# Kernel optimization log

Hardware: AMD Instinct MI355X
Metric: run time of the kernel (lower is better)

Reference implementation:

```python
import jax, jax.numpy as jnp
import numpy as np

N, IN_DIM, H, D = 4096, 512, 8, 64
NEG = -1e9  # additive mask value for non-edges


def setup_inputs() -> dict:
    key = jax.random.key(0)
    k1, k2, k3, k4, k5, k6 = jax.random.split(key, 6)
    data = jax.random.normal(k1, (N, IN_DIM), dtype=jnp.float32)
    r = jax.random.uniform(k2, (N, N), dtype=jnp.float32)
    connectivity = jnp.where(r < 0.05, 0.0, NEG).astype(jnp.float32)
    # xavier-uniform-ish init for params
    lim_w = float(np.sqrt(6.0 / (IN_DIM + H * D)))
    W = jax.random.uniform(k3, (H * D, IN_DIM), jnp.float32, -lim_w, lim_w)
    b = jnp.zeros((H * D,), jnp.float32)
    lim_p = float(np.sqrt(6.0 / (H * D + 1)))
    src_proj = jax.random.uniform(k4, (1, H, D), jnp.float32, -lim_p, lim_p)
    trg_proj = jax.random.uniform(k5, (1, H, D), jnp.float32, -lim_p, lim_p)
    return {"data": data, "connectivity": connectivity, "W": W, "b": b,
            "src_proj": src_proj, "trg_proj": trg_proj}


def reference(data, connectivity, W, b, src_proj, trg_proj):
    # dropout is identity in eval mode (reference is deterministic)
    data1 = (data @ W.T + b).reshape(N, H, D)          # (N,H,D)
    src = jnp.einsum('nhd,xhd->nh', data1, src_proj)   # (N,H)
    trg = jnp.einsum('nhd,xhd->nh', data1, trg_proj)   # (N,H)
    # scores: (H,N,1) + (H,1,N) broadcast outer-sum
    e = src.T[:, :, None] + trg.T[:, None, :]          # (H,N,N)
    e = jnp.where(e >= 0, e, 0.01 * e)                 # LeakyReLU(0.01)
    e = e + connectivity[None, :, :]                   # additive mask
    scores = jax.nn.softmax(e, axis=-1)                # (H,N,N)
    # bmm over heads: (H,N,N) x (H,N,D) -> (H,N,D)
    out = jnp.einsum('hnm,hmd->hnd', scores, data1.transpose(1, 0, 2))
    out = out.transpose(1, 0, 2).reshape(N, H * D)     # concat=True
    return out
```

## Files before the change

### kernel.cpp

```cpp
#include <hip/hip_runtime.h>
#include <hip/hip_bf16.h>

#define NN 4096
#define IN_DIM 512
#define NH 8
#define DD 64
#define HD 512
#define RCAP 448
#define GEMM_WGS 512
#define SCAN_WGS 1024
#define LOG2E 1.4426950408889634f


typedef __attribute__((ext_vector_type(8))) short short8;
typedef __attribute__((ext_vector_type(4))) float f32x4;
typedef __attribute__((ext_vector_type(2))) float f32x2;

static __device__ __forceinline__ unsigned short f2bf(float x) {
    __hip_bfloat16 h = __float2bfloat16(x);
    return *reinterpret_cast<unsigned short*>(&h);
}

__global__ __launch_bounds__(256) void k_cast2(const float* __restrict__ inA,
                                               unsigned short* __restrict__ outA,
                                               int n4A,
                                               const float* __restrict__ inB,
                                               unsigned short* __restrict__ outB,
                                               int n4B) {
    int t = blockIdx.x * 256 + threadIdx.x;
    const float* in;
    unsigned short* out;
    if (t < n4A) {
        in = inA; out = outA;
    } else {
        t -= n4A;
        if (t >= n4B) return;
        in = inB; out = outB;
    }
    float4 v = ((const float4*)in)[t];
    ushort4 o;
    o.x = f2bf(v.x); o.y = f2bf(v.y); o.z = f2bf(v.z); o.w = f2bf(v.w);
    ((ushort4*)out)[t] = o;
}

__global__ __launch_bounds__(256) void k_gemm_scan(const unsigned short* __restrict__ Ab,
                                                   const unsigned short* __restrict__ Wb,
                                                   const float* __restrict__ bias,
                                                   const float* __restrict__ sp,
                                                   const float* __restrict__ tp,
                                                   const float* __restrict__ conn,
                                                   unsigned short* __restrict__ Cb,
                                                   float* __restrict__ src,
                                                   float* __restrict__ trg,
                                                   unsigned long long* __restrict__ bm) {
    const int lane = threadIdx.x & 63;
    const int w = threadIdx.x >> 6;

    if (blockIdx.x >= GEMM_WGS) {
        const int row = (blockIdx.x - GEMM_WGS) * 4 + w;
        const float* crow = conn + (size_t)row * NN;
        unsigned long long keep = 0;
#pragma unroll 8
        for (int t = 0; t < 64; t++) {
            float c = crow[t * 64 + lane];
            unsigned long long m = __ballot(c == 0.0f);
            if (lane == t) keep = m;
        }
        bm[(size_t)row * 64 + lane] = keep;
        return;
    }

    const int col = lane & 15;
    const int quad = lane >> 4;
    const int koff = quad * 8;
    const int h = blockIdx.x & 7;
    const int m0 = h * 64;
    const int n0 = (blockIdx.x >> 3) * 64;

    const short8* ap  = (const short8*)(Ab + (size_t)(n0 + w * 16 + col) * IN_DIM + koff);
    const short8* bp0 = (const short8*)(Wb + (size_t)(m0 +  0 + col) * IN_DIM + koff);
    const short8* bp1 = (const short8*)(Wb + (size_t)(m0 + 16 + col) * IN_DIM + koff);
    const short8* bp2 = (const short8*)(Wb + (size_t)(m0 + 32 + col) * IN_DIM + koff);
    const short8* bp3 = (const short8*)(Wb + (size_t)(m0 + 48 + col) * IN_DIM + koff);

    f32x4 acc0 = {0.f, 0.f, 0.f, 0.f}, acc1 = acc0, acc2 = acc0, acc3 = acc0;

#pragma unroll 4
    for (int ks = 0; ks < 16; ks++) {
        short8 a  = ap[ks * 4];
        short8 b0 = bp0[ks * 4];
        short8 b1 = bp1[ks * 4];
        short8 b2 = bp2[ks * 4];
        short8 b3 = bp3[ks * 4];
        acc0 = __builtin_amdgcn_mfma_f32_16x16x32_bf16(a, b0, acc0, 0, 0, 0);
        acc1 = __builtin_amdgcn_mfma_f32_16x16x32_bf16(a, b1, acc1, 0, 0, 0);
        acc2 = __builtin_amdgcn_mfma_f32_16x16x32_bf16(a, b2, acc2, 0, 0, 0);
        acc3 = __builtin_amdgcn_mfma_f32_16x16x32_bf16(a, b3, acc3, 0, 0, 0);
    }

    const int rbase = n0 + w * 16 + quad * 4;
    f32x4 accs[4] = {acc0, acc1, acc2, acc3};
    float ps[4] = {0.f, 0.f, 0.f, 0.f};
    float pt[4] = {0.f, 0.f, 0.f, 0.f};
#pragma unroll
    for (int mt = 0; mt < 4; mt++) {
        const int m = m0 + mt * 16 + col;
        const float bv  = bias[m];
        const float spv = sp[m];
        const float tpv = tp[m];
#pragma unroll
        for (int r = 0; r < 4; r++) {
            float v = accs[mt][r] + bv;
            Cb[(size_t)(rbase + r) * HD + m] = f2bf(v);
            ps[r] += v * spv;
            pt[r] += v * tpv;
        }
    }
#pragma unroll
    for (int off = 1; off <= 8; off <<= 1) {
#pragma unroll
        for (int r = 0; r < 4; r++) {
            ps[r] += __shfl_xor(ps[r], off, 64);
            pt[r] += __shfl_xor(pt[r], off, 64);
        }
    }
    if (col < 4)
        src[(rbase + col) * 8 + h] = ps[col] * LOG2E;
    else if (col < 8)
        trg[(rbase + col - 4) * 8 + h] = pt[col - 4] * LOG2E;
}

__global__ __launch_bounds__(256) void k_rowattn(const unsigned long long* __restrict__ bm,
                                                 const float* __restrict__ src,
                                                 const float* __restrict__ trg,
                                                 const unsigned short* __restrict__ d1b,
                                                 float* __restrict__ out) {
    __shared__ unsigned short elist[RCAP + 8];
    __shared__ int sTot;
    __shared__ float cbuf[3][64][9];
    const int w = threadIdx.x >> 6, lane = threadIdx.x & 63;
    const int i = blockIdx.x;
    const int h = lane >> 3, d8 = lane & 7;

    if (threadIdx.x < 64) {
        unsigned long long m = bm[(size_t)i * 64 + lane];
        const int cnt = __popcll(m);
        int pre = cnt;
#pragma unroll
        for (int off = 1; off < 64; off <<= 1) {
            int v = __shfl_up(pre, off, 64);
            if (lane >= off) pre += v;
        }
        int tot = __shfl(pre, 63, 64);
        int pos = pre - cnt;
        const int base = lane * 64;
        while (m) {
            int b = __builtin_ctzll(m);
            m &= m - 1;
            if (pos < RCAP) elist[pos] = (unsigned short)(base + b);
            pos++;
        }
        if (tot > RCAP) tot = RCAP;
        unsigned short sv = (tot > 0) ? elist[tot - 1] : (unsigned short)0;
        if (lane < 8) elist[tot + lane] = sv;
        if (lane == 0) sTot = tot;
    }
    __syncthreads();
    const int tot = sTot;

    const float sh = src[i * 8 + h];
    const unsigned voffB = (unsigned)(h * 64 + d8 * 8) * 2u;
    const unsigned toffB = (unsigned)h << 2;
    const unsigned char* vb = (const unsigned char*)d1b;
    const unsigned char* tb = (const unsigned char*)trg;
    const int kbeg = (tot * w) >> 2;
    const int kend = (tot * (w + 1)) >> 2;

    f32x2 a01 = {0.f, 0.f}, a23 = a01, a45 = a01, a67 = a01;
    float lsum = 0.f;
    if (kend > kbeg) {
        unsigned j0 = elist[kbeg];
        unsigned j1 = elist[kbeg + 1];
        unsigned j2 = elist[kbeg + 2];
        float t0 = *(const float*)(tb + (j0 << 5) + toffB);
        float t1 = *(const float*)(tb + (j1 << 5) + toffB);
        uint4 U0 = *(const uint4*)(vb + (j0 << 10) + voffB);
        uint4 U1 = *(const uint4*)(vb + (j1 << 10) + voffB);
#pragma unroll 3
        for (int k = kbeg; k < kend; k++) {
            unsigned j3 = elist[k + 3];
            float t2 = *(const float*)(tb + (j2 << 5) + toffB);
            uint4 U2 = *(const uint4*)(vb + (j2 << 10) + voffB);
            float e = sh + t0;
            e = fmaxf(e, 0.01f * e);
            float p = __builtin_amdgcn_exp2f(e);
            lsum += p;
            f32x2 p2 = {p, p};
            f32x2 v01 = {__uint_as_float(U0.x << 16), __uint_as_float(U0.x & 0xffff0000u)};
            f32x2 v23 = {__uint_as_float(U0.y << 16), __uint_as_float(U0.y & 0xffff0000u)};
            f32x2 v45 = {__uint_as_float(U0.z << 16), __uint_as_float(U0.z & 0xffff0000u)};
            f32x2 v67 = {__uint_as_float(U0.w << 16), __uint_as_float(U0.w & 0xffff0000u)};
            a01 += p2 * v01;
            a23 += p2 * v23;
            a45 += p2 * v45;
            a67 += p2 * v67;
            t0 = t1; t1 = t2;
            U0 = U1; U1 = U2;
            j2 = j3;
        }
    }

    float acc[8] = {a01.x, a01.y, a23.x, a23.y, a45.x, a45.y, a67.x, a67.y};
    if (w > 0) {
#pragma unroll
        for (int r = 0; r < 8; r++) cbuf[w - 1][lane][r] = acc[r];
        cbuf[w - 1][lane][8] = lsum;
    }
    __syncthreads();
    if (w == 0) {
#pragma unroll
        for (int wv = 0; wv < 3; wv++) {
#pragma unroll
            for (int r = 0; r < 8; r++) acc[r] += cbuf[wv][lane][r];
            lsum += cbuf[wv][lane][8];
        }
        float inv = (lsum > 0.f) ? (1.f / lsum) : 0.f;
        float* op = out + (size_t)i * HD + h * 64 + d8 * 8;
        *(float4*)op = make_float4(acc[0] * inv, acc[1] * inv, acc[2] * inv, acc[3] * inv);
        *(float4*)(op + 4) = make_float4(acc[4] * inv, acc[5] * inv, acc[6] * inv, acc[7] * inv);
    }
}

extern "C" void kernel_launch(void* const* d_in, const int* in_sizes, int n_in,
                              void* d_out, int out_size, void* d_ws, size_t ws_size,
                              hipStream_t stream) {
    const float* data = (const float*)d_in[0];
    const float* conn = (const float*)d_in[1];
    const float* W    = (const float*)d_in[2];
    const float* bias = (const float*)d_in[3];
    const float* sp   = (const float*)d_in[4];
    const float* tp   = (const float*)d_in[5];
    float* out = (float*)d_out;

    unsigned short* d1b = (unsigned short*)d_ws;
    unsigned short* Ab  = d1b + (size_t)NN * HD;
    unsigned short* Wb  = Ab + (size_t)NN * IN_DIM;
    float* src  = (float*)(Wb + (size_t)HD * IN_DIM);
    float* trg  = src + NN * NH;
    unsigned long long* bm = (unsigned long long*)(trg + NN * NH);

    const int n4A = NN * IN_DIM / 4;
    const int n4B = HD * IN_DIM / 4;
    k_cast2<<<dim3((n4A + n4B + 255) / 256), 256, 0, stream>>>(data, Ab, n4A, W, Wb, n4B);
    k_gemm_scan<<<dim3(GEMM_WGS + SCAN_WGS), 256, 0, stream>>>(Ab, Wb, bias, sp, tp, conn,
                                                               d1b, src, trg, bm);
    k_rowattn<<<dim3(NN), 256, 0, stream>>>(bm, src, trg, d1b, out);
}
```

Baseline: 169.0 us.

## Replace sparse per-row gather attention with dense bitmask-masked MFMA flash attention

Drops the per-row edge-list gather kernel. A dense flash-style kernel now walks all 4096 columns in tiles of 32, builds the mask from the bitmask, computes exp2 scores, packs them to bf16 and accumulates P·V with bf16 MFMA. To give that kernel contiguous loads, the projection GEMM writes its features and the src/trg scores in head-major transposed layouts. The connectivity bitmask scan moves into the cast kernel instead of running alongside the GEMM. This trades the latency-bound scattered gathers for regular tensor-core work, but it does roughly twenty times more exp and MAC work (every non-edge is computed), re-reads the whole value matrix in every workgroup, and launches only 256 workgroups.

```diff
diff --git a/kernel.cpp b/kernel.cpp
--- a/kernel.cpp
+++ b/kernel.cpp
@@ -6,27 +6,43 @@
 #define NH 8
 #define DD 64
 #define HD 512
-#define RCAP 448
-#define GEMM_WGS 512
+#define LOG2E 1.4426950408889634f
+#define CAST_WGS 2304
 #define SCAN_WGS 1024
-#define LOG2E 1.4426950408889634f
+#define FLASH_WGS 256
 
 
 typedef __attribute__((ext_vector_type(8))) short short8;
 typedef __attribute__((ext_vector_type(4))) float f32x4;
-typedef __attribute__((ext_vector_type(2))) float f32x2;
 
 static __device__ __forceinline__ unsigned short f2bf(float x) {
     __hip_bfloat16 h = __float2bfloat16(x);
     return *reinterpret_cast<unsigned short*>(&h);
 }
 
-__global__ __launch_bounds__(256) void k_cast2(const float* __restrict__ inA,
-                                               unsigned short* __restrict__ outA,
-                                               int n4A,
-                                               const float* __restrict__ inB,
-                                               unsigned short* __restrict__ outB,
-                                               int n4B) {
+__global__ __launch_bounds__(256) void k_cast_scan(const float* __restrict__ inA,
+                                                   unsigned short* __restrict__ outA,
+                                                   int n4A,
+                                                   const float* __restrict__ inB,
+                                                   unsigned short* __restrict__ outB,
+                                                   int n4B,
+                                                   const float* __restrict__ conn,
+                                                   unsigned long long* __restrict__ bm) {
+    if (blockIdx.x >= CAST_WGS) {
+        const int lane = threadIdx.x & 63;
+        const int w = threadIdx.x >> 6;
+        const int row = (blockIdx.x - CAST_WGS) * 4 + w;
+        const float* crow = conn + (size_t)row * NN;
+        unsigned long long keep = 0;
+#pragma unroll 8
+        for (int t = 0; t < 64; t++) {
+            float c = crow[t * 64 + lane];
+            unsigned long long m = __ballot(c == 0.0f);
+            if (lane == t) keep = m;
+        }
+        bm[(size_t)row * 64 + lane] = keep;
+        return;
+    }
     int t = blockIdx.x * 256 + threadIdx.x;
     const float* in;
     unsigned short* out;
@@ -43,39 +59,22 @@
     ((ushort4*)out)[t] = o;
 }
 
-__global__ __launch_bounds__(256) void k_gemm_scan(const unsigned short* __restrict__ Ab,
-                                                   const unsigned short* __restrict__ Wb,
-                                                   const float* __restrict__ bias,
-                                                   const float* __restrict__ sp,
-                                                   const float* __restrict__ tp,
-                                                   const float* __restrict__ conn,
-                                                   unsigned short* __restrict__ Cb,
-                                                   float* __restrict__ src,
-                                                   float* __restrict__ trg,
-                                                   unsigned long long* __restrict__ bm) {
+__global__ __launch_bounds__(256) void k_gemm_fused(const unsigned short* __restrict__ Ab,
+                                                    const unsigned short* __restrict__ Wb,
+                                                    const float* __restrict__ bias,
+                                                    const float* __restrict__ sp,
+                                                    const float* __restrict__ tp,
+                                                    unsigned short* __restrict__ d1t,
+                                                    float* __restrict__ srcT,
+                                                    float* __restrict__ trgT) {
     const int lane = threadIdx.x & 63;
     const int w = threadIdx.x >> 6;
-
-    if (blockIdx.x >= GEMM_WGS) {
-        const int row = (blockIdx.x - GEMM_WGS) * 4 + w;
-        const float* crow = conn + (size_t)row * NN;
-        unsigned long long keep = 0;
-#pragma unroll 8
-        for (int t = 0; t < 64; t++) {
-            float c = crow[t * 64 + lane];
-            unsigned long long m = __ballot(c == 0.0f);
-            if (lane == t) keep = m;
-        }
-        bm[(size_t)row * 64 + lane] = keep;
-        return;
-    }
-
     const int col = lane & 15;
     const int quad = lane >> 4;
     const int koff = quad * 8;
-    const int h = blockIdx.x & 7;
+    const int h = blockIdx.x;
     const int m0 = h * 64;
-    const int n0 = (blockIdx.x >> 3) * 64;
+    const int n0 = blockIdx.y * 64;
 
     const short8* ap  = (const short8*)(Ab + (size_t)(n0 + w * 16 + col) * IN_DIM + koff);
     const short8* bp0 = (const short8*)(Wb + (size_t)(m0 +  0 + col) * IN_DIM + koff);
@@ -108,13 +107,16 @@
         const float bv  = bias[m];
         const float spv = sp[m];
         const float tpv = tp[m];
+        ushort4 pack;
+        unsigned short* pk = (unsigned short*)&pack;
 #pragma unroll
         for (int r = 0; r < 4; r++) {
             float v = accs[mt][r] + bv;
-            Cb[(size_t)(rbase + r) * HD + m] = f2bf(v);
+            pk[r] = f2bf(v);
             ps[r] += v * spv;
             pt[r] += v * tpv;
         }
+        *(ushort4*)(d1t + (size_t)m * NN + rbase) = pack;
     }
 #pragma unroll
     for (int off = 1; off <= 8; off <<= 1) {
@@ -125,109 +127,112 @@
         }
     }
     if (col < 4)
-        src[(rbase + col) * 8 + h] = ps[col] * LOG2E;
+        srcT[(size_t)h * NN + rbase + col] = ps[col] * LOG2E;
     else if (col < 8)
-        trg[(rbase + col - 4) * 8 + h] = pt[col - 4] * LOG2E;
-}
-
-__global__ __launch_bounds__(256) void k_rowattn(const unsigned long long* __restrict__ bm,
-                                                 const float* __restrict__ src,
-                                                 const float* __restrict__ trg,
-                                                 const unsigned short* __restrict__ d1b,
-                                                 float* __restrict__ out) {
-    __shared__ unsigned short elist[RCAP + 8];
-    __shared__ int sTot;
-    __shared__ float cbuf[3][64][9];
-    const int w = threadIdx.x >> 6, lane = threadIdx.x & 63;
-    const int i = blockIdx.x;
-    const int h = lane >> 3, d8 = lane & 7;
-
-    if (threadIdx.x < 64) {
-        unsigned long long m = bm[(size_t)i * 64 + lane];
-        const int cnt = __popcll(m);
-        int pre = cnt;
-#pragma unroll
-        for (int off = 1; off < 64; off <<= 1) {
-            int v = __shfl_up(pre, off, 64);
-            if (lane >= off) pre += v;
-        }
-        int tot = __shfl(pre, 63, 64);
-        int pos = pre - cnt;
-        const int base = lane * 64;
-        while (m) {
-            int b = __builtin_ctzll(m);
-            m &= m - 1;
-            if (pos < RCAP) elist[pos] = (unsigned short)(base + b);
-            pos++;
-        }
-        if (tot > RCAP) tot = RCAP;
-        unsigned short sv = (tot > 0) ? elist[tot - 1] : (unsigned short)0;
-        if (lane < 8) elist[tot + lane] = sv;
-        if (lane == 0) sTot = tot;
-    }
-    __syncthreads();
-    const int tot = sTot;
-
-    const float sh = src[i * 8 + h];
-    const unsigned voffB = (unsigned)(h * 64 + d8 * 8) * 2u;
-    const unsigned toffB = (unsigned)h << 2;
-    const unsigned char* vb = (const unsigned char*)d1b;
-    const unsigned char* tb = (const unsigned char*)trg;
-    const int kbeg = (tot * w) >> 2;
-    const int kend = (tot * (w + 1)) >> 2;
-
-    f32x2 a01 = {0.f, 0.f}, a23 = a01, a45 = a01, a67 = a01;
-    float lsum = 0.f;
-    if (kend > kbeg) {
-        unsigned j0 = elist[kbeg];
-        unsigned j1 = elist[kbeg + 1];
-        unsigned j2 = elist[kbeg + 2];
-        float t0 = *(const float*)(tb + (j0 << 5) + toffB);
-        float t1 = *(const float*)(tb + (j1 << 5) + toffB);
-        uint4 U0 = *(const uint4*)(vb + (j0 << 10) + voffB);
-        uint4 U1 = *(const uint4*)(vb + (j1 << 10) + voffB);
-#pragma unroll 3
-        for (int k = kbeg; k < kend; k++) {
-            unsigned j3 = elist[k + 3];
-            float t2 = *(const float*)(tb + (j2 << 5) + toffB);
-            uint4 U2 = *(const uint4*)(vb + (j2 << 10) + voffB);
-            float e = sh + t0;
-            e = fmaxf(e, 0.01f * e);
-            float p = __builtin_amdgcn_exp2f(e);
-            lsum += p;
-            f32x2 p2 = {p, p};
-            f32x2 v01 = {__uint_as_float(U0.x << 16), __uint_as_float(U0.x & 0xffff0000u)};
-            f32x2 v23 = {__uint_as_float(U0.y << 16), __uint_as_float(U0.y & 0xffff0000u)};
-            f32x2 v45 = {__uint_as_float(U0.z << 16), __uint_as_float(U0.z & 0xffff0000u)};
-            f32x2 v67 = {__uint_as_float(U0.w << 16), __uint_as_float(U0.w & 0xffff0000u)};
-            a01 += p2 * v01;
-            a23 += p2 * v23;
-            a45 += p2 * v45;
-            a67 += p2 * v67;
-            t0 = t1; t1 = t2;
-            U0 = U1; U1 = U2;
-            j2 = j3;
-        }
-    }
-
-    float acc[8] = {a01.x, a01.y, a23.x, a23.y, a45.x, a45.y, a67.x, a67.y};
-    if (w > 0) {
-#pragma unroll
-        for (int r = 0; r < 8; r++) cbuf[w - 1][lane][r] = acc[r];
-        cbuf[w - 1][lane][8] = lsum;
-    }
-    __syncthreads();
-    if (w == 0) {
-#pragma unroll
-        for (int wv = 0; wv < 3; wv++) {
-#pragma unroll
-            for (int r = 0; r < 8; r++) acc[r] += cbuf[wv][lane][r];
-            lsum += cbuf[wv][lane][8];
-        }
-        float inv = (lsum > 0.f) ? (1.f / lsum) : 0.f;
-        float* op = out + (size_t)i * HD + h * 64 + d8 * 8;
-        *(float4*)op = make_float4(acc[0] * inv, acc[1] * inv, acc[2] * inv, acc[3] * inv);
-        *(float4*)(op + 4) = make_float4(acc[4] * inv, acc[5] * inv, acc[6] * inv, acc[7] * inv);
+        trgT[(size_t)h * NN + rbase + col - 4] = pt[col - 4] * LOG2E;
+}
+
+__global__ __launch_bounds__(256) void k_flash(const unsigned* __restrict__ bm32,
+                                               const float* __restrict__ srcT,
+                                               const float* __restrict__ trgT,
+                                               const unsigned short* __restrict__ d1t,
+                                               float* __restrict__ out) {
+    const int lane = threadIdx.x & 63;
+    const int w = threadIdx.x >> 6;
+    const int col = lane & 15;
+    const int kq = lane >> 4;
+    const int i0 = blockIdx.x * 16;
+    const int h0 = w * 2;
+    const int m = i0 + col;
+    const int sh0 = kq * 8;
+
+    const float s0 = srcT[(size_t)h0 * NN + m];
+    const float s1 = srcT[(size_t)(h0 + 1) * NN + m];
+    const unsigned* bp = bm32 + (size_t)m * 128;
+    const float* tp0 = trgT + (size_t)h0 * NN + sh0;
+    const float* tp1 = tp0 + NN;
+    const short8* vp[2][4];
+#pragma unroll
+    for (int hh = 0; hh < 2; hh++)
+#pragma unroll
+        for (int dt = 0; dt < 4; dt++)
+            vp[hh][dt] = (const short8*)(d1t +
+                (size_t)((h0 + hh) * 64 + dt * 16 + col) * NN + sh0);
+
+    f32x4 acc[2][4];
+#pragma unroll
+    for (int hh = 0; hh < 2; hh++)
+#pragma unroll
+        for (int dt = 0; dt < 4; dt++)
+            acc[hh][dt] = (f32x4){0.f, 0.f, 0.f, 0.f};
+    float ds0 = 0.f, ds1 = 0.f;
+
+#pragma unroll 2
+    for (int jt = 0; jt < 128; jt++) {
+        const unsigned bw = bp[jt];
+        const float4 ta = *(const float4*)(tp0 + jt * 32);
+        const float4 tb = *(const float4*)(tp0 + jt * 32 + 4);
+        const float4 tc = *(const float4*)(tp1 + jt * 32);
+        const float4 td = *(const float4*)(tp1 + jt * 32 + 4);
+        short8 v00 = vp[0][0][jt * 4];
+        short8 v01 = vp[0][1][jt * 4];
+        short8 v02 = vp[0][2][jt * 4];
+        short8 v03 = vp[0][3][jt * 4];
+        short8 v10 = vp[1][0][jt * 4];
+        short8 v11 = vp[1][1][jt * 4];
+        short8 v12 = vp[1][2][jt * 4];
+        short8 v13 = vp[1][3][jt * 4];
+
+        const float t0a[8] = {ta.x, ta.y, ta.z, ta.w, tb.x, tb.y, tb.z, tb.w};
+        const float t1a[8] = {tc.x, tc.y, tc.z, tc.w, td.x, td.y, td.z, td.w};
+        float p0[8], p1[8];
+#pragma unroll
+        for (int r = 0; r < 8; r++) {
+            unsigned b = (bw >> (sh0 + r)) & 1u;
+            float msk = __uint_as_float((b - 1u) & 0xC3480000u);
+            float e0 = s0 + t0a[r];
+            e0 = fmaxf(e0, 0.01f * e0) + msk;
+            p0[r] = __builtin_amdgcn_exp2f(e0);
+            ds0 += p0[r];
+            float e1 = s1 + t1a[r];
+            e1 = fmaxf(e1, 0.01f * e1) + msk;
+            p1[r] = __builtin_amdgcn_exp2f(e1);
+            ds1 += p1[r];
+        }
+        short8 pa0, pa1;
+#pragma unroll
+        for (int r = 0; r < 8; r++) {
+            pa0[r] = (short)f2bf(p0[r]);
+            pa1[r] = (short)f2bf(p1[r]);
+        }
+        acc[0][0] = __builtin_amdgcn_mfma_f32_16x16x32_bf16(pa0, v00, acc[0][0], 0, 0, 0);
+        acc[0][1] = __builtin_amdgcn_mfma_f32_16x16x32_bf16(pa0, v01, acc[0][1], 0, 0, 0);
+        acc[0][2] = __builtin_amdgcn_mfma_f32_16x16x32_bf16(pa0, v02, acc[0][2], 0, 0, 0);
+        acc[0][3] = __builtin_amdgcn_mfma_f32_16x16x32_bf16(pa0, v03, acc[0][3], 0, 0, 0);
+        acc[1][0] = __builtin_amdgcn_mfma_f32_16x16x32_bf16(pa1, v10, acc[1][0], 0, 0, 0);
+        acc[1][1] = __builtin_amdgcn_mfma_f32_16x16x32_bf16(pa1, v11, acc[1][1], 0, 0, 0);
+        acc[1][2] = __builtin_amdgcn_mfma_f32_16x16x32_bf16(pa1, v12, acc[1][2], 0, 0, 0);
+        acc[1][3] = __builtin_amdgcn_mfma_f32_16x16x32_bf16(pa1, v13, acc[1][3], 0, 0, 0);
+    }
+
+    ds0 += __shfl_xor(ds0, 16, 64);
+    ds0 += __shfl_xor(ds0, 32, 64);
+    ds1 += __shfl_xor(ds1, 16, 64);
+    ds1 += __shfl_xor(ds1, 32, 64);
+
+#pragma unroll
+    for (int r = 0; r < 4; r++) {
+        const int row = i0 + kq * 4 + r;
+        float d0 = __shfl(ds0, kq * 4 + r, 64);
+        float d1 = __shfl(ds1, kq * 4 + r, 64);
+        float inv0 = (d0 > 0.f) ? (1.f / d0) : 0.f;
+        float inv1 = (d1 > 0.f) ? (1.f / d1) : 0.f;
+        float* op = out + (size_t)row * HD + h0 * 64;
+#pragma unroll
+        for (int dt = 0; dt < 4; dt++) {
+            op[dt * 16 + col]      = acc[0][dt][r] * inv0;
+            op[64 + dt * 16 + col] = acc[1][dt][r] * inv1;
+        }
     }
 }
 
@@ -242,17 +247,18 @@
     const float* tp   = (const float*)d_in[5];
     float* out = (float*)d_out;
 
-    unsigned short* d1b = (unsigned short*)d_ws;
-    unsigned short* Ab  = d1b + (size_t)NN * HD;
+    unsigned short* d1t = (unsigned short*)d_ws;
+    unsigned short* Ab  = d1t + (size_t)HD * NN;
     unsigned short* Wb  = Ab + (size_t)NN * IN_DIM;
-    float* src  = (float*)(Wb + (size_t)HD * IN_DIM);
-    float* trg  = src + NN * NH;
-    unsigned long long* bm = (unsigned long long*)(trg + NN * NH);
+    float* srcT = (float*)(Wb + (size_t)HD * IN_DIM);
+    float* trgT = srcT + NH * NN;
+    unsigned long long* bm = (unsigned long long*)(trgT + NH * NN);
 
     const int n4A = NN * IN_DIM / 4;
     const int n4B = HD * IN_DIM / 4;
-    k_cast2<<<dim3((n4A + n4B + 255) / 256), 256, 0, stream>>>(data, Ab, n4A, W, Wb, n4B);
-    k_gemm_scan<<<dim3(GEMM_WGS + SCAN_WGS), 256, 0, stream>>>(Ab, Wb, bias, sp, tp, conn,
-                                                               d1b, src, trg, bm);
-    k_rowattn<<<dim3(NN), 256, 0, stream>>>(bm, src, trg, d1b, out);
-}
+    k_cast_scan<<<dim3(CAST_WGS + SCAN_WGS), 256, 0, stream>>>(data, Ab, n4A, W, Wb, n4B,
+                                                               conn, bm);
+    k_gemm_fused<<<dim3(NH, NN / 64), 256, 0, stream>>>(Ab, Wb, bias, sp, tp,
+                                                        d1t, srcT, trgT);
+    k_flash<<<dim3(FLASH_WGS), 256, 0, stream>>>((const unsigned*)bm, srcT, trgT, d1t, out);
+}
```

Result: slower. 386.5 us (+128.7%).
